# Kernel tuning notes

Measured on AMD Instinct MI355X. Metric: run time of the kernel, lower is better.

Reference implementation:

```python
import jax, jax.numpy as jnp
import numpy as np

SKIP = 2
EPS = 1e-9
K_PEN = 0.01
MU_BG = 0.0
VAR_BG = 100.0
SIZ = (256, 256, 256)
SIZA = (160, 192, 160)
NC = 10
COMPS = np.array([2, 2, 1, 1, 2, 1, 1, 2, 1])
NG = int(COMPS.sum())  # 13
FSIZ = (13, 13, 13)  # round(256*1.0/20)


def setup_inputs() -> dict:
    key = jax.random.key(0)
    ks = jax.random.split(key, 10)
    I = jax.random.uniform(ks[0], SIZ, jnp.float32)
    A = jax.random.uniform(ks[1], (*SIZA, NC), jnp.float32)
    A = A / jnp.sum(A, axis=-1, keepdims=True)  # probabilistic atlas
    aff_I = jnp.eye(4, dtype=jnp.float32)
    aff_A = jnp.diag(jnp.array([SIZ[0] / SIZA[0], SIZ[1] / SIZA[1], SIZ[2] / SIZA[2], 1.0], jnp.float32))
    mus = jax.random.uniform(ks[2], (NG,), jnp.float32)
    vars_ = 0.05 + 0.1 * jax.random.uniform(ks[3], (NG,), jnp.float32)
    w = np.asarray(jax.random.uniform(ks[4], (NG,))) + 0.1
    cls = np.repeat(np.arange(len(COMPS)), COMPS)
    onehot = (cls[:, None] == np.arange(len(COMPS))[None, :]).astype(np.float32)
    w = w / (onehot @ (onehot.T @ w))  # weights sum to 1 within each class
    weights = jnp.asarray(w, jnp.float32)
    gmm_onehot = jnp.asarray(onehot)
    ts = 0.5 * jax.random.normal(ks[5], (3,), jnp.float32)
    thetas = 2.0 * jax.random.normal(ks[6], (3,), jnp.float32)  # degrees
    scalings = 0.5 * jax.random.normal(ks[7], (3,), jnp.float32)
    shears = 0.5 * jax.random.normal(ks[8], (3,), jnp.float32)
    FIELD = 0.5 * jax.random.normal(ks[9], (*FSIZ, 3), jnp.float32)
    return dict(I=I, A=A, aff_I=aff_I, aff_A=aff_A, mus=mus, vars_=vars_, weights=weights,
                gmm_onehot=gmm_onehot, ts=ts, thetas=thetas, scalings=scalings,
                shears=shears, FIELD=FIELD)


def _bspline3(t):
    t = jnp.abs(t)
    return jnp.where(t < 1, (4.0 - 6.0 * t * t + 3.0 * t * t * t) / 6.0,
                     jnp.where(t < 2, (2.0 - t) ** 3 / 6.0, 0.0))


def _cubic_matrix(coords, n):
    # dense [m, n] cubic-B-spline sampling matrix with circular (dft) boundary,
    # prefilter=False (FIELD values treated as spline coefficients)
    m = coords.shape[0]
    base = jnp.floor(coords).astype(jnp.int32)
    W = jnp.zeros((m, n), coords.dtype)
    rows = jnp.arange(m)
    for k in (-1, 0, 1, 2):
        node = base + k
        W = W.at[rows, node % n].add(_bspline3(coords - node))
    return W


def reference(I, A, aff_I, aff_A, mus, vars_, weights, gmm_onehot, ts, thetas, scalings, shears, FIELD):
    nxA, nyA, nzA, C = A.shape
    fx, fy, fz = FIELD.shape[:3]
    dt = I.dtype

    # ---- affine from parameters (T @ Sh @ Sc @ Rz @ Ry @ Rx) ----
    th = thetas * (jnp.pi / 180.0)
    sh = shears / 100.0
    sc = jnp.exp(scalings / 20.0)
    c, s = jnp.cos(th), jnp.sin(th)
    Rx = jnp.array([[1.0, 0.0, 0.0, 0.0], [0.0, c[0], -s[0], 0.0], [0.0, s[0], c[0], 0.0], [0.0, 0.0, 0.0, 1.0]])
    Ry = jnp.array([[c[1], 0.0, s[1], 0.0], [0.0, 1.0, 0.0, 0.0], [-s[1], 0.0, c[1], 0.0], [0.0, 0.0, 0.0, 1.0]])
    Rz = jnp.array([[c[2], -s[2], 0.0, 0.0], [s[2], c[2], 0.0, 0.0], [0.0, 0.0, 1.0, 0.0], [0.0, 0.0, 0.0, 1.0]])
    Sc = jnp.diag(jnp.concatenate([sc, jnp.ones((1,), sc.dtype)]))
    Sh = jnp.array([[1.0, sh[1], sh[2], 0.0], [sh[0], 1.0, sh[2], 0.0], [sh[0], sh[1], 1.0, 0.0], [0.0, 0.0, 0.0, 1.0]])
    T = jnp.eye(4, dtype=dt).at[:3, 3].set(ts)
    AFF = T @ Sh @ Sc @ Rz @ Ry @ Rx
    V = jnp.linalg.inv(AFF @ aff_A) @ aff_I  # image voxel -> atlas voxel

    # ---- cubic-spline resample of deformation field (separable grid) ----
    xs = jnp.arange(0, I.shape[0], SKIP).astype(dt)
    ys = jnp.arange(0, I.shape[1], SKIP).astype(dt)
    zs = jnp.arange(0, I.shape[2], SKIP).astype(dt)
    field_f = FIELD / 100.0 * jnp.array([nxA, nyA, nzA], dt)  # [fx,fy,fz,3]
    Wx = _cubic_matrix(fx * xs / I.shape[0], fx)
    Wy = _cubic_matrix(fy * ys / I.shape[1], fy)
    Wz = _cubic_matrix(fz * zs / I.shape[2], fz)
    t1 = jnp.einsum('ia,abcd->ibcd', Wx, field_f)
    t1 = jnp.einsum('jb,ibcd->ijcd', Wy, t1)
    field_rs = jnp.einsum('kc,ijcd->ijkd', Wz, t1)  # [X,Y,Z,3]

    X = xs[:, None, None]
    Y = ys[None, :, None]
    Z = zs[None, None, :]
    gx = V[0, 0] * X + V[0, 1] * Y + V[0, 2] * Z + V[0, 3] + field_rs[..., 0]
    gy = V[1, 0] * X + V[1, 1] * Y + V[1, 2] * Z + V[1, 3] + field_rs[..., 1]
    gz = V[2, 0] * X + V[2, 1] * Y + V[2, 2] * Z + V[2, 3] + field_rs[..., 2]

    # ---- trilinear pull of atlas (zero bound, no extrapolation) ----
    x0 = jnp.floor(gx).astype(jnp.int32); rx = gx - x0
    y0 = jnp.floor(gy).astype(jnp.int32); ry = gy - y0
    z0 = jnp.floor(gz).astype(jnp.int32); rz = gz - z0
    Af = A.reshape(-1, C)
    acc = jnp.zeros((*gx.shape, C), dt)
    for dx in (0, 1):
        ix = x0 + dx; wx = rx if dx else 1.0 - rx
        vx = (ix >= 0) & (ix < nxA); ixc = jnp.clip(ix, 0, nxA - 1)
        for dy in (0, 1):
            iy = y0 + dy; wy = ry if dy else 1.0 - ry
            vy = (iy >= 0) & (iy < nyA); iyc = jnp.clip(iy, 0, nyA - 1)
            for dz in (0, 1):
                iz = z0 + dz; wz = rz if dz else 1.0 - rz
                vz = (iz >= 0) & (iz < nzA); izc = jnp.clip(iz, 0, nzA - 1)
                w = jnp.where(vx & vy & vz, wx * wy * wz, 0.0)
                flat = (ixc * nyA + iyc) * nzA + izc
                vals = jnp.take(Af, flat.reshape(-1), axis=0).reshape(*flat.shape, C)
                acc = acc + w[..., None] * vals

    atlas_rs = jnp.clip(acc, 0.0, 1.0)
    missing = 1.0 - jnp.sum(atlas_rs, axis=-1)
    prior_bg = jnp.clip(atlas_rs[..., 0] + missing, 0.0, 1.0)
    priors_rest = atlas_rs[..., 1:]  # already clipped to [0,1]
    priors = jnp.concatenate([prior_bg[..., None], priors_rest], axis=-1)

    # ---- GMM likelihoods ----
    Iskip = I[::SKIP, ::SKIP, ::SKIP]
    gl_bg = jnp.exp(-0.5 * (Iskip - MU_BG) ** 2 / VAR_BG) / jnp.sqrt(2.0 * jnp.pi * VAR_BG)
    gl = jnp.exp(-0.5 * (Iskip[..., None] - mus) ** 2 / vars_) / jnp.sqrt(2.0 * jnp.pi * vars_)  # [X,Y,Z,NG]
    class_lh = jnp.einsum('xyzg,gc->xyzc', weights * gl, gmm_onehot)  # per-class mixture
    normalizer = prior_bg * gl_bg + jnp.sum(priors_rest * class_lh, axis=-1)
    log_lh = jnp.log(EPS + normalizer)

    # ---- gradient penalty on field in voxel units of the full image grid ----
    siz_vec = jnp.array(I.shape, dt)
    fsiz_vec = jnp.array(FIELD.shape[:3], dt)
    fv = field_f * (fsiz_vec / siz_vec)
    pen = (jnp.mean((fv[1:] - fv[:-1]) ** 2)
           + jnp.mean((fv[:, 1:] - fv[:, :-1]) ** 2)
           + jnp.mean((fv[:, :, 1:] - fv[:, :, :-1]) ** 2)) / 3.0
    def_pen = K_PEN * pen
    loss = -jnp.mean(log_lh) + def_pen
    grids_new = jnp.stack([gx, gy, gz], axis=-1)
    return (loss, grids_new, priors, def_pen)
```

## Files before the change

kernel.cpp:

```cpp
#include <hip/hip_runtime.h>

#define PI_D 3.14159265358979323846
#define NS 128
#define NVOX (NS*NS*NS)
#define NBLK (NVOX/256)

typedef float f4v __attribute__((ext_vector_type(4)));
typedef f4v f4u __attribute__((aligned(8)));
typedef float f4s __attribute__((ext_vector_type(4), aligned(4)));


static __device__ __forceinline__ float bspline3f(float t) {
    t = fabsf(t);
    if (t < 1.0f) return (4.0f - 6.0f*t*t + 3.0f*t*t*t) * (1.0f/6.0f);
    if (t < 2.0f) { float u = 2.0f - t; return u*u*u * (1.0f/6.0f); }
    return 0.0f;
}

static __device__ void mm4(const double* Am, const double* Bm, double* Cm) {
    for (int i = 0; i < 4; i++)
        for (int j = 0; j < 4; j++) {
            double s = 0.0;
            for (int k = 0; k < 4; k++) s += Am[i*4+k] * Bm[k*4+j];
            Cm[i*4+j] = s;
        }
}

static __device__ void inv4(const double* Am, double* Om) {
    double a[4][8];
    for (int i = 0; i < 4; i++)
        for (int j = 0; j < 4; j++) {
            a[i][j]   = Am[i*4+j];
            a[i][4+j] = (i == j) ? 1.0 : 0.0;
        }
    for (int col = 0; col < 4; col++) {
        int piv = col; double best = fabs(a[col][col]);
        for (int r = col+1; r < 4; r++) {
            double v = fabs(a[r][col]);
            if (v > best) { best = v; piv = r; }
        }
        if (piv != col)
            for (int j = 0; j < 8; j++) { double t = a[col][j]; a[col][j] = a[piv][j]; a[piv][j] = t; }
        double d = a[col][col];
        for (int j = 0; j < 8; j++) a[col][j] /= d;
        for (int r = 0; r < 4; r++) if (r != col) {
            double f = a[r][col];
            for (int j = 0; j < 8; j++) a[r][j] -= f * a[col][j];
        }
    }
    for (int i = 0; i < 4; i++)
        for (int j = 0; j < 4; j++) Om[i*4+j] = a[i][4+j];
}


__global__ void AD_prep(const float* __restrict__ aff_I, const float* __restrict__ aff_A,
                        const float* __restrict__ ts, const float* __restrict__ thetas,
                        const float* __restrict__ scalings, const float* __restrict__ shears,
                        const float* __restrict__ FIELD,
                        const float* __restrict__ vars_, const float* __restrict__ weights,
                        const float* __restrict__ mus,
                        float* __restrict__ wsf, int* __restrict__ wsi)
{
    const int tid = threadIdx.x;

    if (tid == 0) {
        double c0 = cos((double)thetas[0]*(PI_D/180.0)), s0 = sin((double)thetas[0]*(PI_D/180.0));
        double c1 = cos((double)thetas[1]*(PI_D/180.0)), s1 = sin((double)thetas[1]*(PI_D/180.0));
        double c2 = cos((double)thetas[2]*(PI_D/180.0)), s2 = sin((double)thetas[2]*(PI_D/180.0));
        double Rx[16] = {1,0,0,0,  0,c0,-s0,0,  0,s0,c0,0,  0,0,0,1};
        double Ry[16] = {c1,0,s1,0,  0,1,0,0,  -s1,0,c1,0,  0,0,0,1};
        double Rz[16] = {c2,-s2,0,0,  s2,c2,0,0,  0,0,1,0,  0,0,0,1};
        double t1[16], t2[16];
        mm4(Ry, Rx, t1);
        mm4(Rz, t1, t2);
        double sc0 = exp((double)scalings[0]/20.0);
        double sc1 = exp((double)scalings[1]/20.0);
        double sc2 = exp((double)scalings[2]/20.0);
        for (int j = 0; j < 4; j++) { t2[0*4+j] *= sc0; t2[1*4+j] *= sc1; t2[2*4+j] *= sc2; }
        double sh0 = (double)shears[0]/100.0, sh1 = (double)shears[1]/100.0, sh2 = (double)shears[2]/100.0;
        double Sh[16] = {1,sh1,sh2,0,  sh0,1,sh2,0,  sh0,sh1,1,0,  0,0,0,1};
        mm4(Sh, t2, t1);
        t1[3]  += (double)ts[0];
        t1[7]  += (double)ts[1];
        t1[11] += (double)ts[2];
        double Aa[16]; for (int i = 0; i < 16; i++) Aa[i] = (double)aff_A[i];
        mm4(t1, Aa, t2);
        double Mi[16]; inv4(t2, Mi);
        double Ai[16]; for (int i = 0; i < 16; i++) Ai[i] = (double)aff_I[i];
        mm4(Mi, Ai, t1);
        for (int i = 0; i < 16; i++) wsf[i] = (float)t1[i];
    }

    if (tid < 13) {
        float va = vars_[tid];
        wsf[17+tid] = weights[tid] / sqrtf(6.283185307179586f * va);
        wsf[32+tid] = -0.5f / va;
        wsf[48+tid] = mus[tid];
    }

    if (tid < 128) {
        for (int a = 0; a < 3; a++) {
            float coord = (13.0f * (float)(2*tid)) / 256.0f;
            int base = (int)floorf(coord);
            for (int k = 0; k < 4; k++) {
                int node = base + (k - 1);
                float w = bspline3f(coord - (float)node);
                int idx = node % 13; if (idx < 0) idx += 13;
                wsf[64 + (a*128+tid)*4 + k] = w;
                wsi[(a*128+tid)*4 + k] = idx;
            }
        }
    }

    __shared__ double red[256];
    double s = 0.0;
    for (int i = tid; i < 12*13*13*3; i += 256) {
        int d = i % 3; int r = i / 3; int cc = r % 13; r /= 13; int b = r % 13; int a = r / 13;
        float sf = (d == 1) ? 0.0975f : 0.08125f;
        float f1 = FIELD[(((a+1)*13+b)*13+cc)*3+d] * sf;
        float f0 = FIELD[(((a  )*13+b)*13+cc)*3+d] * sf;
        float df = f1 - f0; s += (double)(df*df);
    }
    for (int i = tid; i < 13*12*13*3; i += 256) {
        int d = i % 3; int r = i / 3; int cc = r % 13; r /= 13; int b = r % 12; int a = r / 12;
        float sf = (d == 1) ? 0.0975f : 0.08125f;
        float f1 = FIELD[((a*13+(b+1))*13+cc)*3+d] * sf;
        float f0 = FIELD[((a*13+(b  ))*13+cc)*3+d] * sf;
        float df = f1 - f0; s += (double)(df*df);
    }
    for (int i = tid; i < 13*13*12*3; i += 256) {
        int d = i % 3; int r = i / 3; int cc = r % 12; r /= 12; int b = r % 13; int a = r / 13;
        float sf = (d == 1) ? 0.0975f : 0.08125f;
        float f1 = FIELD[((a*13+b)*13+(cc+1))*3+d] * sf;
        float f0 = FIELD[((a*13+b)*13+(cc  ))*3+d] * sf;
        float df = f1 - f0; s += (double)(df*df);
    }
    red[tid] = s; __syncthreads();
    for (int st = 128; st > 0; st >>= 1) {
        if (tid < st) red[tid] += red[tid+st];
        __syncthreads();
    }
    if (tid == 0) wsf[16] = (float)(0.01 * red[0] / (6084.0 * 3.0));
}

__global__ void AD_field(const float* __restrict__ FIELD,
                         const float* __restrict__ wsf, const int* __restrict__ wsi,
                         float* __restrict__ tB)
{
    __shared__ float fld[13*13*13*3];
    const int tid = threadIdx.x;
    for (int i = tid; i < 13*13*13*3; i += 256) {
        int d = i - (i/3)*3;
        float sc = (d == 1) ? 1.92f : 1.6f;
        fld[i] = FIELD[i] * sc;
    }
    __syncthreads();

    const int p = blockIdx.x*256 + tid;
    const int j = p & 127, i = p >> 7;

    const float4 wx = *(const float4*)(wsf + 64 + (0*128+i)*4);
    const float4 wy = *(const float4*)(wsf + 64 + (1*128+j)*4);
    const int4  ix4 = *(const int4*)(wsi + (0*128+i)*4);
    const int4  iy4 = *(const int4*)(wsi + (1*128+j)*4);
    const float wxa[4] = {wx.x, wx.y, wx.z, wx.w};
    const float wya[4] = {wy.x, wy.y, wy.z, wy.w};
    const int   ixa[4] = {ix4.x, ix4.y, ix4.z, ix4.w};
    const int   iya[4] = {iy4.x, iy4.y, iy4.z, iy4.w};

    float acc[39];
    #pragma unroll
    for (int t = 0; t < 39; t++) acc[t] = 0.f;

    #pragma unroll
    for (int a = 0; a < 4; a++) {
        #pragma unroll
        for (int b = 0; b < 4; b++) {
            const float wab = wxa[a] * wya[b];
            const float* src = fld + (ixa[a]*13 + iya[b]) * 39;
            #pragma unroll
            for (int t = 0; t < 39; t++) acc[t] = fmaf(wab, src[t], acc[t]);
        }
    }
    float* dst = tB + (size_t)p * 39;
    #pragma unroll
    for (int t = 0; t < 39; t++) dst[t] = acc[t];
}

__launch_bounds__(256)
__global__ void AD_main(const float* __restrict__ I, const float* __restrict__ A,
                        const float* __restrict__ wsf, const int* __restrict__ wsi,
                        const float* __restrict__ tB,
                        double* __restrict__ partials, float* __restrict__ out)
{
    __shared__ float sh[80];
    __shared__ double wred[4];
    __shared__ __align__(16) float sg[768];
    __shared__ __align__(16) float sp[2560];
    const int tid = threadIdx.x;

    const int wg = ((blockIdx.x & 7) << 10) + (blockIdx.x >> 3);

    {
        const float* src = tB + (size_t)(wg * 2) * 39;
        if (tid < 78) sh[tid] = src[tid];
    }
    __syncthreads();

    const int v = wg*256 + tid;
    const int z = v & 127, y = (v >> 7) & 127, x = v >> 14;

    const float4 wzv = *(const float4*)(wsf + 64 + (2*128+z)*4);
    const int4  izv = *(const int4*)(wsi + (2*128+z)*4);
    const float* myrow = sh + (tid >> 7) * 39;

    float fr0, fr1, fr2;
    {
        const float* r0 = myrow + izv.x*3;
        const float* r1 = myrow + izv.y*3;
        const float* r2 = myrow + izv.z*3;
        const float* r3 = myrow + izv.w*3;
        fr0 = wzv.x*r0[0] + wzv.y*r1[0] + wzv.z*r2[0] + wzv.w*r3[0];
        fr1 = wzv.x*r0[1] + wzv.y*r1[1] + wzv.z*r2[1] + wzv.w*r3[1];
        fr2 = wzv.x*r0[2] + wzv.y*r1[2] + wzv.z*r2[2] + wzv.w*r3[2];
    }

    const float X = (float)(2*x), Yf = (float)(2*y), Zf = (float)(2*z);
    const float gx = wsf[0]*X + wsf[1]*Yf + wsf[2]*Zf  + wsf[3]  + fr0;
    const float gy = wsf[4]*X + wsf[5]*Yf + wsf[6]*Zf  + wsf[7]  + fr1;
    const float gz = wsf[8]*X + wsf[9]*Yf + wsf[10]*Zf + wsf[11] + fr2;

    sg[tid*3+0] = gx; sg[tid*3+1] = gy; sg[tid*3+2] = gz;

    const float x0f = floorf(gx), y0f = floorf(gy), z0f = floorf(gz);
    const int x0 = (int)x0f, y0 = (int)y0f, z0 = (int)z0f;
    const float rx = gx - x0f, ry = gy - y0f, rz = gz - z0f;

    int lx[2], ly[2]; float wxt[2], wyt[2], wzt[2];
    lx[0] = x0   < 0 ? 0 : (x0   > 159 ? 159 : x0);
    lx[1] = x0+1 < 0 ? 0 : (x0+1 > 159 ? 159 : x0+1);
    ly[0] = y0   < 0 ? 0 : (y0   > 191 ? 191 : y0);
    ly[1] = y0+1 < 0 ? 0 : (y0+1 > 191 ? 191 : y0+1);
    wxt[0] = (x0   >= 0 && x0   < 160) ? (1.f - rx) : 0.f;
    wxt[1] = (x0+1 >= 0 && x0+1 < 160) ? rx : 0.f;
    wyt[0] = (y0   >= 0 && y0   < 192) ? (1.f - ry) : 0.f;
    wyt[1] = (y0+1 >= 0 && y0+1 < 192) ? ry : 0.f;
    wzt[0] = (z0   >= 0 && z0   < 160) ? (1.f - rz) : 0.f;
    wzt[1] = (z0+1 >= 0 && z0+1 < 160) ? rz : 0.f;

    const int zb = z0 < 0 ? 0 : (z0 > 158 ? 158 : z0);
    const bool hi0 = (z0 >= 159);
    const bool lo1 = (z0 < 0);

    float acc[10];
    #pragma unroll
    for (int c = 0; c < 10; c++) acc[c] = 0.f;

    #pragma unroll
    for (int ta = 0; ta < 2; ta++) {
        #pragma unroll
        for (int tb = 0; tb < 2; tb++) {
            const float wab = wxt[ta] * wyt[tb];
            const float w0 = wab * wzt[0];
            const float w1 = wab * wzt[1];
            const f4u* p = (const f4u*)(A + ((size_t)(lx[ta]*192 + ly[tb])*160 + zb)*10);
            const f4v L0 = p[0], L1 = p[1], L2 = p[2], L3 = p[3], L4 = p[4];
            const float lo[10] = {L0.x,L0.y,L0.z,L0.w, L1.x,L1.y,L1.z,L1.w, L2.x,L2.y};
            const float hiv[10] = {L2.z,L2.w, L3.x,L3.y,L3.z,L3.w, L4.x,L4.y,L4.z,L4.w};
            #pragma unroll
            for (int c = 0; c < 10; c++) {
                const float t0 = hi0 ? hiv[c] : lo[c];
                const float t1 = lo1 ? lo[c]  : hiv[c];
                acc[c] = fmaf(w0, t0, acc[c]);
                acc[c] = fmaf(w1, t1, acc[c]);
            }
        }
    }

    float pri[10]; float sum = 0.f;
    #pragma unroll
    for (int c = 0; c < 10; c++) {
        float t = acc[c]; t = t < 0.f ? 0.f : (t > 1.f ? 1.f : t);
        pri[c] = t; sum += t;
    }
    float p0 = pri[0] + (1.0f - sum);
    pri[0] = p0 < 0.f ? 0.f : (p0 > 1.f ? 1.f : p0);

    #pragma unroll
    for (int c = 0; c < 10; c++) sp[tid*10+c] = pri[c];

    const float Iv = __builtin_nontemporal_load(I + ((size_t)(2*x)*256 + (size_t)(2*y))*256 + (size_t)(2*z));
    const float gl_bg = expf(-0.005f*Iv*Iv) * 0.039894228040143274f;

    constexpr int CLS[13] = {0,0,1,1,2,3,4,4,5,6,7,7,8};
    float lh[9];
    #pragma unroll
    for (int c = 0; c < 9; c++) lh[c] = 0.f;
    #pragma unroll
    for (int g = 0; g < 13; g++) {
        const float dlt = Iv - wsf[48+g];
        lh[CLS[g]] += wsf[17+g] * expf(dlt*dlt*wsf[32+g]);
    }
    float nrm = pri[0] * gl_bg;
    #pragma unroll
    for (int c = 0; c < 9; c++) nrm = fmaf(pri[c+1], lh[c], nrm);
    const float ll = logf(1e-9f + nrm);

    double s = (double)ll;
    #pragma unroll
    for (int off = 32; off > 0; off >>= 1) s += __shfl_down(s, off, 64);
    if ((tid & 63) == 0) wred[tid >> 6] = s;
    __syncthreads();
    if (tid == 0) partials[wg] = (wred[0] + wred[1]) + (wred[2] + wred[3]);

    {
        const f4s* g4 = (const f4s*)sg;
        f4s* gdst = (f4s*)(out + 1) + (size_t)wg*192;
        if (tid < 192) __builtin_nontemporal_store(g4[tid], gdst + tid);

        const f4s* p4 = (const f4s*)sp;
        f4s* pdst = (f4s*)(out + 1 + (size_t)NVOX*3) + (size_t)wg*640;
        #pragma unroll
        for (int k = 0; k < 3; k++) {
            int j = k*256 + tid;
            if (j < 640) __builtin_nontemporal_store(p4[j], pdst + j);
        }
    }
}

__global__ void AD_fin(const double* __restrict__ partials, const float* __restrict__ wsf,
                       float* __restrict__ out, int out_size)
{
    __shared__ double red[256];
    const int tid = threadIdx.x;
    double s = 0.0;
    for (int i = tid; i < NBLK; i += 256) s += partials[i];
    red[tid] = s; __syncthreads();
    for (int st = 128; st > 0; st >>= 1) {
        if (tid < st) red[tid] += red[tid+st];
        __syncthreads();
    }
    if (tid == 0) {
        float dp = wsf[16];
        out[0] = (float)(-(red[0] / (double)NVOX) + (double)dp);
        out[out_size-1] = dp;
    }
}

extern "C" void kernel_launch(void* const* d_in, const int* in_sizes, int n_in,
                              void* d_out, int out_size, void* d_ws, size_t ws_size,
                              hipStream_t stream)
{
    const float* I        = (const float*)d_in[0];
    const float* A        = (const float*)d_in[1];
    const float* aff_I    = (const float*)d_in[2];
    const float* aff_A    = (const float*)d_in[3];
    const float* mus      = (const float*)d_in[4];
    const float* vars_    = (const float*)d_in[5];
    const float* weights  = (const float*)d_in[6];
    const float* ts       = (const float*)d_in[8];
    const float* thetas   = (const float*)d_in[9];
    const float* scalings = (const float*)d_in[10];
    const float* shears   = (const float*)d_in[11];
    const float* FIELD    = (const float*)d_in[12];

    float* out = (float*)d_out;
    float* wsf = (float*)d_ws;
    int*   wsi = (int*)(wsf + 1600);
    double* partials = (double*)((char*)d_ws + 16384);
    float* tB = (float*)((char*)d_ws + 131072);

    hipLaunchKernelGGL(AD_prep, dim3(1), dim3(256), 0, stream,
                       aff_I, aff_A, ts, thetas, scalings, shears, FIELD, vars_, weights, mus, wsf, wsi);
    hipLaunchKernelGGL(AD_field, dim3(64), dim3(256), 0, stream,
                       FIELD, wsf, wsi, tB);
    hipLaunchKernelGGL(AD_main, dim3(NBLK), dim3(256), 0, stream,
                       I, A, wsf, wsi, tB, partials, out);
    hipLaunchKernelGGL(AD_fin, dim3(1), dim3(256), 0, stream,
                       partials, wsf, out, out_size);
}
```

Before: 116.8 us.

## Process two voxels per thread and realign output stores to 16-byte vectors

```diff
diff --git a/kernel.cpp b/kernel.cpp
--- a/kernel.cpp
+++ b/kernel.cpp
@@ -3,11 +3,10 @@
 #define PI_D 3.14159265358979323846
 #define NS 128
 #define NVOX (NS*NS*NS)
-#define NBLK (NVOX/256)
+#define NBLK (NVOX/512)
 
 typedef float f4v __attribute__((ext_vector_type(4)));
 typedef f4v f4u __attribute__((aligned(8)));
-typedef float f4s __attribute__((ext_vector_type(4), aligned(4)));
 
 
 static __device__ __forceinline__ float bspline3f(float t) {
@@ -187,32 +186,14 @@
     for (int t = 0; t < 39; t++) dst[t] = acc[t];
 }
 
-__launch_bounds__(256)
-__global__ void AD_main(const float* __restrict__ I, const float* __restrict__ A,
-                        const float* __restrict__ wsf, const int* __restrict__ wsi,
-                        const float* __restrict__ tB,
-                        double* __restrict__ partials, float* __restrict__ out)
-{
-    __shared__ float sh[80];
-    __shared__ double wred[4];
-    __shared__ __align__(16) float sg[768];
-    __shared__ __align__(16) float sp[2560];
-    const int tid = threadIdx.x;
-
-    const int wg = ((blockIdx.x & 7) << 10) + (blockIdx.x >> 3);
-
-    {
-        const float* src = tB + (size_t)(wg * 2) * 39;
-        if (tid < 78) sh[tid] = src[tid];
-    }
-    __syncthreads();
-
-    const int v = wg*256 + tid;
-    const int z = v & 127, y = (v >> 7) & 127, x = v >> 14;
-
+static __device__ __forceinline__ void voxel_compute(
+    int x, int y, int z, const float* __restrict__ myrow,
+    const float* __restrict__ wsf, const int* __restrict__ wsi,
+    const float* __restrict__ I, const float* __restrict__ A,
+    float* __restrict__ g3, float* __restrict__ pri, float* __restrict__ llp)
+{
     const float4 wzv = *(const float4*)(wsf + 64 + (2*128+z)*4);
     const int4  izv = *(const int4*)(wsi + (2*128+z)*4);
-    const float* myrow = sh + (tid >> 7) * 39;
 
     float fr0, fr1, fr2;
     {
@@ -229,8 +210,7 @@
     const float gx = wsf[0]*X + wsf[1]*Yf + wsf[2]*Zf  + wsf[3]  + fr0;
     const float gy = wsf[4]*X + wsf[5]*Yf + wsf[6]*Zf  + wsf[7]  + fr1;
     const float gz = wsf[8]*X + wsf[9]*Yf + wsf[10]*Zf + wsf[11] + fr2;
-
-    sg[tid*3+0] = gx; sg[tid*3+1] = gy; sg[tid*3+2] = gz;
+    g3[0] = gx; g3[1] = gy; g3[2] = gz;
 
     const float x0f = floorf(gx), y0f = floorf(gy), z0f = floorf(gz);
     const int x0 = (int)x0f, y0 = (int)y0f, z0 = (int)z0f;
@@ -277,7 +257,7 @@
         }
     }
 
-    float pri[10]; float sum = 0.f;
+    float sum = 0.f;
     #pragma unroll
     for (int c = 0; c < 10; c++) {
         float t = acc[c]; t = t < 0.f ? 0.f : (t > 1.f ? 1.f : t);
@@ -286,9 +266,6 @@
     float p0 = pri[0] + (1.0f - sum);
     pri[0] = p0 < 0.f ? 0.f : (p0 > 1.f ? 1.f : p0);
 
-    #pragma unroll
-    for (int c = 0; c < 10; c++) sp[tid*10+c] = pri[c];
-
     const float Iv = __builtin_nontemporal_load(I + ((size_t)(2*x)*256 + (size_t)(2*y))*256 + (size_t)(2*z));
     const float gl_bg = expf(-0.005f*Iv*Iv) * 0.039894228040143274f;
 
@@ -304,9 +281,47 @@
     float nrm = pri[0] * gl_bg;
     #pragma unroll
     for (int c = 0; c < 9; c++) nrm = fmaf(pri[c+1], lh[c], nrm);
-    const float ll = logf(1e-9f + nrm);
-
-    double s = (double)ll;
+    *llp = logf(1e-9f + nrm);
+}
+
+__launch_bounds__(256)
+__global__ void AD_main(const float* __restrict__ I, const float* __restrict__ A,
+                        const float* __restrict__ wsf, const int* __restrict__ wsi,
+                        const float* __restrict__ tB,
+                        double* __restrict__ partials, float* __restrict__ out)
+{
+    __shared__ float sh[160];
+    __shared__ double wred[4];
+    __shared__ __align__(16) float sgbuf[1537];
+    __shared__ __align__(16) float spbuf[5121];
+    float* sg = sgbuf + 1;
+    float* sp = spbuf + 1;
+    const int tid = threadIdx.x;
+
+    const int wg = ((blockIdx.x & 7) << 9) + (blockIdx.x >> 3);
+
+    {
+        const float* src = tB + (size_t)(wg * 4) * 39;
+        if (tid < 156) sh[tid] = src[tid];
+    }
+    __syncthreads();
+
+    const int r = tid >> 6, z0l = tid & 63;
+    const int vbase = wg*512 + r*128;
+    const int y = (vbase >> 7) & 127, x = vbase >> 14;
+    const float* myrow = sh + r*39;
+
+    float g0[3], g1[3], p0a[10], p1a[10], ll0, ll1;
+    voxel_compute(x, y, z0l,      myrow, wsf, wsi, I, A, g0, p0a, &ll0);
+    voxel_compute(x, y, z0l + 64, myrow, wsf, wsi, I, A, g1, p1a, &ll1);
+
+    const int i0 = r*128 + z0l, i1 = i0 + 64;
+    #pragma unroll
+    for (int c = 0; c < 3; c++)  { sg[i0*3+c]  = g0[c];  sg[i1*3+c]  = g1[c]; }
+    #pragma unroll
+    for (int c = 0; c < 10; c++) { sp[i0*10+c] = p0a[c]; sp[i1*10+c] = p1a[c]; }
+
+    double s = (double)ll0 + (double)ll1;
     #pragma unroll
     for (int off = 32; off > 0; off >>= 1) s += __shfl_down(s, off, 64);
     if ((tid & 63) == 0) wred[tid >> 6] = s;
@@ -314,16 +329,25 @@
     if (tid == 0) partials[wg] = (wred[0] + wred[1]) + (wred[2] + wred[3]);
 
     {
-        const f4s* g4 = (const f4s*)sg;
-        f4s* gdst = (f4s*)(out + 1) + (size_t)wg*192;
-        if (tid < 192) __builtin_nontemporal_store(g4[tid], gdst + tid);
-
-        const f4s* p4 = (const f4s*)sp;
-        f4s* pdst = (f4s*)(out + 1 + (size_t)NVOX*3) + (size_t)wg*640;
+        float* gbase = out + 1 + (size_t)wg*1536;
+        if (tid < 3) __builtin_nontemporal_store(sg[tid], gbase + tid);
+        if (tid == 3) __builtin_nontemporal_store(sg[1535], gbase + 1535);
+        const f4v* g4 = (const f4v*)(sg + 3);
+        f4v* gdst = (f4v*)(gbase + 3);
+        if (tid < 256) {
+            __builtin_nontemporal_store(g4[tid], gdst + tid);
+            int j = 256 + tid;
+            if (j < 383) __builtin_nontemporal_store(g4[j], gdst + j);
+        }
+        float* pbase = out + 1 + (size_t)NVOX*3 + (size_t)wg*5120;
+        if (tid < 3) __builtin_nontemporal_store(sp[tid], pbase + tid);
+        if (tid == 3) __builtin_nontemporal_store(sp[5119], pbase + 5119);
+        const f4v* p4 = (const f4v*)(sp + 3);
+        f4v* pdst = (f4v*)(pbase + 3);
         #pragma unroll
-        for (int k = 0; k < 3; k++) {
+        for (int k = 0; k < 5; k++) {
             int j = k*256 + tid;
-            if (j < 640) __builtin_nontemporal_store(p4[j], pdst + j);
+            if (j < 1279) __builtin_nontemporal_store(p4[j], pdst + j);
         }
     }
 }
```

New measurement: 122.6 us. 1.05x slower.
